# Optimization experiments

Hardware: AMD Instinct MI355X
Metric: run time of the kernel (lower is better)

Reference implementation:

```python
import jax, jax.numpy as jnp
import numpy as np

S, B, I, H = 512, 8192, 3, 5  # seq, batch, input_size, hidden_size


def _uniform(key, shape, bound):
    return jax.random.uniform(key, shape, jnp.float32, -bound, bound)


def setup_inputs() -> dict:
    key = jax.random.key(0)
    ks = jax.random.split(key, 17)
    bound = 1.0 / np.sqrt(H)
    inp = {"x": jax.random.normal(ks[0], (S, B, I), jnp.float32)}
    # layer 0: in=I ; layer 1: in=2H (concat of both directions). Suffix 'r' = reverse direction.
    specs = [
        ("l0", I), ("l0r", I), ("l1", 2 * H), ("l1r", 2 * H),
    ]
    ki = 1
    for name, din in specs:
        inp[f"w_ih_{name}"] = _uniform(ks[ki], (4 * H, din), bound); ki += 1
        inp[f"w_hh_{name}"] = _uniform(ks[ki], (4 * H, H), bound); ki += 1
        inp[f"b_ih_{name}"] = _uniform(ks[ki], (4 * H,), bound); ki += 1
        inp[f"b_hh_{name}"] = _uniform(ks[ki], (4 * H,), bound); ki += 1
    return inp


def _lstm_dir(x, w_ih, w_hh, b_ih, b_hh, reverse):
    """Single-direction LSTM over x [S,B,Din] -> (hs [S,B,H], h_T [B,H], c_T [B,H])."""
    xs = x[::-1] if reverse else x
    # Precompute input contributions for all timesteps in one big matmul.
    gx = jnp.einsum('sbi,gi->sbg', xs, w_ih) + b_ih + b_hh  # [S,B,4H]
    h0 = jnp.zeros((x.shape[1], H), x.dtype)
    c0 = jnp.zeros((x.shape[1], H), x.dtype)

    def step(carry, g):
        h, c = carry
        g = g + h @ w_hh.T  # [B,4H]
        i, f, gg, o = jnp.split(g, 4, axis=-1)  # PyTorch gate order: i,f,g,o
        i = jax.nn.sigmoid(i)
        f = jax.nn.sigmoid(f)
        gg = jnp.tanh(gg)
        o = jax.nn.sigmoid(o)
        c = f * c + i * gg
        h = o * jnp.tanh(c)
        return (h, c), h

    (hT, cT), hs = jax.lax.scan(step, (h0, c0), gx)
    if reverse:
        hs = hs[::-1]
    return hs, hT, cT


def reference(x,
              w_ih_l0, w_hh_l0, b_ih_l0, b_hh_l0,
              w_ih_l0r, w_hh_l0r, b_ih_l0r, b_hh_l0r,
              w_ih_l1, w_hh_l1, b_ih_l1, b_hh_l1,
              w_ih_l1r, w_hh_l1r, b_ih_l1r, b_hh_l1r):
    # Layer 0 (bidirectional)
    hs0f, h0f, c0f = _lstm_dir(x, w_ih_l0, w_hh_l0, b_ih_l0, b_hh_l0, False)
    hs0b, h0b, c0b = _lstm_dir(x, w_ih_l0r, w_hh_l0r, b_ih_l0r, b_hh_l0r, True)
    out0 = jnp.concatenate([hs0f, hs0b], axis=-1)  # [S,B,2H]
    # Layer 1 (bidirectional) consumes concat of both directions
    hs1f, h1f, c1f = _lstm_dir(out0, w_ih_l1, w_hh_l1, b_ih_l1, b_hh_l1, False)
    hs1b, h1b, c1b = _lstm_dir(out0, w_ih_l1r, w_hh_l1r, b_ih_l1r, b_hh_l1r, True)
    output = jnp.concatenate([hs1f, hs1b], axis=-1)  # [S,B,2H]
    # PyTorch h_n/c_n layout: [num_layers*num_directions, B, H] ordered (l0 fwd, l0 bwd, l1 fwd, l1 bwd)
    h_n = jnp.stack([h0f, h0b, h1f, h1b], axis=0)
    c_n = jnp.stack([c0f, c0b, c1f, c1b], axis=0)
    return output, h_n, c_n
```

## Files before the change

kernel.cpp:

```cpp
#include <hip/hip_runtime.h>


constexpr int S_ = 512;
constexpr int B_ = 8192;
constexpr int NROW = 16384;

constexpr float L2E  = 1.4426950408889634f;
constexpr float T2E  = 2.8853900817779268f;
constexpr float IT2E = 0.34657359027997264f;

typedef _Float16 v2h __attribute__((ext_vector_type(2)));

__device__ __forceinline__ float dot2h(v2h a, v2h b, float c) {
#if __has_builtin(__builtin_amdgcn_fdot2)
    return __builtin_amdgcn_fdot2(a, b, c, false);
#else
    return fmaf((float)a[0], (float)b[0], fmaf((float)a[1], (float)b[1], c));
#endif
}

__device__ __forceinline__ float rcp_(float x) { return __builtin_amdgcn_rcpf(x); }

__device__ __forceinline__ float exp2_(float x) {
#if __has_builtin(__builtin_amdgcn_exp2f)
    return __builtin_amdgcn_exp2f(x);
#else
    return exp2f(x);
#endif
}

__device__ __forceinline__ void sbar() { __builtin_amdgcn_sched_barrier(0); }

__device__ __forceinline__ float bperm(int bidx, float v) {
    return __int_as_float(__builtin_amdgcn_ds_bpermute(bidx, __float_as_int(v)));
}

__device__ __forceinline__ unsigned pkh(float a, float b) {
    auto t = __builtin_amdgcn_cvt_pkrtz(a, b);
    unsigned q; __builtin_memcpy(&q, &t, 4); return q;
}

__global__ __launch_bounds__(64) __attribute__((amdgpu_waves_per_eu(1, 2)))
void lstm_layer0(
    const float* __restrict__ x,
    const float* __restrict__ wih_f, const float* __restrict__ whh_f,
    const float* __restrict__ bih_f, const float* __restrict__ bhh_f,
    const float* __restrict__ wih_r, const float* __restrict__ whh_r,
    const float* __restrict__ bih_r, const float* __restrict__ bhh_r,
    unsigned short* __restrict__ ws,
    float* __restrict__ outbase)
{
    const int l64 = threadIdx.x & 63;
    int r = l64 / 5; r = (r > 11) ? 11 : r;
    const int u   = l64 - r * 5;
    const int uc  = (u < 5) ? u : 4;
    const int gid = blockIdx.x * 12 + r;
    const bool valid = gid < NROW;
    const int dir = (gid >> 13) & 1;
    const int b   = gid & 8191;
    const bool stw = valid && (u < 3);
    const bool st  = valid && (u < 5);

    int bidx[5];
#pragma unroll
    for (int k = 0; k < 5; k++) bidx[k] = (r * 5 + k) * 4;

    const float* __restrict__ wih = dir ? wih_r : wih_f;
    const float* __restrict__ whh = dir ? whh_r : whh_f;
    const float* __restrict__ bih = dir ? bih_r : bih_f;
    const float* __restrict__ bhh = dir ? bhh_r : bhh_f;

    const int rows[4] = {uc, 5 + uc, 10 + uc, 15 + uc};
    const float scl[4] = {-L2E, -L2E, T2E, -L2E};
    float WX[4][3], WH[4][5], BS[4];
#pragma unroll
    for (int gi = 0; gi < 4; gi++) {
        const int rr = rows[gi]; const float sc = scl[gi];
#pragma unroll
        for (int i = 0; i < 3; i++) WX[gi][i] = wih[rr * 3 + i] * sc;
#pragma unroll
        for (int k = 0; k < 5; k++) WH[gi][k] = whh[rr * 5 + k] * sc;
        BS[gi] = (bih[rr] + bhh[rr]) * sc;
    }

    float h[5] = {0.f, 0.f, 0.f, 0.f, 0.f};
    float cp = 0.f, hu_last = 0.f;

    const int t0 = dir ? (S_ - 1) : 0;
    const float* xp = x + ((size_t)t0 * B_ + b) * 3;
    unsigned short* wp = ws + (size_t)dir * ((size_t)S_ * B_ * 6)
                            + ((size_t)t0 * B_ + b) * 6;
    const ptrdiff_t xst = dir ? -(ptrdiff_t)3 * B_ : (ptrdiff_t)3 * B_;
    const ptrdiff_t wst = dir ? -(ptrdiff_t)6 * B_ : (ptrdiff_t)6 * B_;

    auto step = [&](const float (&xin)[3], unsigned short* wpp) {
        float a0 = BS[0], a1 = BS[1], a2 = BS[2], a3 = BS[3];
#pragma unroll
        for (int i = 0; i < 3; i++) {
            a0 = fmaf(WX[0][i], xin[i], a0);
            a1 = fmaf(WX[1][i], xin[i], a1);
            a2 = fmaf(WX[2][i], xin[i], a2);
            a3 = fmaf(WX[3][i], xin[i], a3);
        }
#pragma unroll
        for (int k = 0; k < 5; k++) {
            a0 = fmaf(WH[0][k], h[k], a0);
            a1 = fmaf(WH[1][k], h[k], a1);
            a2 = fmaf(WH[2][k], h[k], a2);
            a3 = fmaf(WH[3][k], h[k], a3);
        }
        const float ig = rcp_(1.0f + exp2_(a0));
        const float fg = rcp_(1.0f + exp2_(a1));
        const float g2 = fmaf(-2.0f * T2E, rcp_(1.0f + exp2_(a2)), T2E);
        const float og = rcp_(1.0f + exp2_(a3));
        cp = fmaf(fg, cp, ig * g2);
        const float th = fmaf(-2.0f, rcp_(1.0f + exp2_(cp)), 1.0f);
        const float hu = og * th;
        hu_last = hu;
#pragma unroll
        for (int k = 0; k < 5; k++) h[k] = bperm(bidx[k], hu);
        const unsigned q0 = pkh(h[0], h[1]);
        const unsigned q1 = pkh(h[2], h[3]);
        const unsigned q2 = pkh(h[4], 0.0f);
        unsigned qs = q0;
        qs = (u == 1) ? q1 : qs;
        qs = (u == 2) ? q2 : qs;
        if (stw) ((unsigned*)wpp)[u] = qs;
    };

    auto ld = [&](float (&buf)[3]) {
        __builtin_memcpy(&buf[0], xp, 12);
        xp += xst;
        sbar();
    };

    float x0[3], x1[3], x2[3], x3[3], x4[3], x5[3], x6[3], x7[3];
    ld(x0); ld(x1); ld(x2); ld(x3); ld(x4); ld(x5); ld(x6); ld(x7);

#pragma unroll 1
    for (int s = 0; s < S_ - 8; s += 8) {
        step(x0, wp); wp += wst; ld(x0);
        step(x1, wp); wp += wst; ld(x1);
        step(x2, wp); wp += wst; ld(x2);
        step(x3, wp); wp += wst; ld(x3);
        step(x4, wp); wp += wst; ld(x4);
        step(x5, wp); wp += wst; ld(x5);
        step(x6, wp); wp += wst; ld(x6);
        step(x7, wp); wp += wst; ld(x7);
    }
    step(x0, wp); wp += wst;
    step(x1, wp); wp += wst;
    step(x2, wp); wp += wst;
    step(x3, wp); wp += wst;
    step(x4, wp); wp += wst;
    step(x5, wp); wp += wst;
    step(x6, wp); wp += wst;
    step(x7, wp);

    const size_t OUTE = (size_t)S_ * B_ * 10;
    float* hn = outbase + OUTE + ((size_t)dir * B_ + b) * 5;
    float* cn = hn + (size_t)4 * B_ * 5;
    if (st) { hn[uc] = hu_last; cn[uc] = cp * IT2E; }
}

__global__ __launch_bounds__(64) __attribute__((amdgpu_waves_per_eu(1, 2)))
void lstm_layer1(
    const unsigned short* __restrict__ ws,
    const float* __restrict__ wih_f, const float* __restrict__ whh_f,
    const float* __restrict__ bih_f, const float* __restrict__ bhh_f,
    const float* __restrict__ wih_r, const float* __restrict__ whh_r,
    const float* __restrict__ bih_r, const float* __restrict__ bhh_r,
    float* __restrict__ outbase)
{
    const int l64 = threadIdx.x & 63;
    int r = l64 / 5; r = (r > 11) ? 11 : r;
    const int u   = l64 - r * 5;
    const int uc  = (u < 5) ? u : 4;
    const int gid = blockIdx.x * 12 + r;
    const bool valid = gid < NROW;
    const int dir = (gid >> 13) & 1;
    const int b   = gid & 8191;
    const bool st = valid && (u < 5);

    int bidx[5];
#pragma unroll
    for (int k = 0; k < 5; k++) bidx[k] = (r * 5 + k) * 4;

    const float* __restrict__ wih = dir ? wih_r : wih_f;
    const float* __restrict__ whh = dir ? whh_r : whh_f;
    const float* __restrict__ bih = dir ? bih_r : bih_f;
    const float* __restrict__ bhh = dir ? bhh_r : bhh_f;

    const int rows[4] = {uc, 5 + uc, 10 + uc, 15 + uc};
    const float scl[4] = {-L2E, -L2E, T2E, -L2E};
    v2h WX[4][6];
    float WH[4][5], BS[4];
#pragma unroll
    for (int gi = 0; gi < 4; gi++) {
        const int rr = rows[gi]; const float sc = scl[gi];
#pragma unroll
        for (int p = 0; p < 6; p++) {
            const int i0 = (p < 3) ? 2 * p : 2 * p - 1;
            const bool pad = (p == 2) || (p == 5);
            const float w0 = wih[rr * 10 + i0] * sc;
            const float w1 = pad ? 0.f : wih[rr * 10 + i0 + 1] * sc;
            WX[gi][p] = (v2h){(_Float16)w0, (_Float16)w1};
        }
#pragma unroll
        for (int k = 0; k < 5; k++) WH[gi][k] = whh[rr * 5 + k] * sc;
        BS[gi] = (bih[rr] + bhh[rr]) * sc;
    }

    float h[5] = {0.f, 0.f, 0.f, 0.f, 0.f};
    float cp = 0.f, hu_last = 0.f;

    const int t0 = dir ? (S_ - 1) : 0;
    const unsigned short* rpf = ws + ((size_t)t0 * B_ + b) * 6;
    const unsigned short* rpb = rpf + (size_t)S_ * B_ * 6;
    float* op = outbase + ((size_t)t0 * B_ + b) * 10 + dir * 5;
    const ptrdiff_t rst = dir ? -(ptrdiff_t)6 * B_ : (ptrdiff_t)6 * B_;
    const ptrdiff_t ost = dir ? -(ptrdiff_t)10 * B_ : (ptrdiff_t)10 * B_;

    auto step = [&](const v2h (&xin)[6], float* opp) {
        float a0 = BS[0], a1 = BS[1], a2 = BS[2], a3 = BS[3];
#pragma unroll
        for (int p = 0; p < 6; p++) {
            a0 = dot2h(xin[p], WX[0][p], a0);
            a1 = dot2h(xin[p], WX[1][p], a1);
            a2 = dot2h(xin[p], WX[2][p], a2);
            a3 = dot2h(xin[p], WX[3][p], a3);
        }
#pragma unroll
        for (int k = 0; k < 5; k++) {
            a0 = fmaf(WH[0][k], h[k], a0);
            a1 = fmaf(WH[1][k], h[k], a1);
            a2 = fmaf(WH[2][k], h[k], a2);
            a3 = fmaf(WH[3][k], h[k], a3);
        }
        const float ig = rcp_(1.0f + exp2_(a0));
        const float fg = rcp_(1.0f + exp2_(a1));
        const float g2 = fmaf(-2.0f * T2E, rcp_(1.0f + exp2_(a2)), T2E);
        const float og = rcp_(1.0f + exp2_(a3));
        cp = fmaf(fg, cp, ig * g2);
        const float th = fmaf(-2.0f, rcp_(1.0f + exp2_(cp)), 1.0f);
        const float hu = og * th;
        hu_last = hu;
        if (st) opp[u] = hu;
#pragma unroll
        for (int k = 0; k < 5; k++) h[k] = bperm(bidx[k], hu);
    };

    auto ld = [&](v2h (&buf)[6]) {
        __builtin_memcpy(&buf[0], rpf, 12);
        __builtin_memcpy(&buf[3], rpb, 12);
        rpf += rst; rpb += rst;
        sbar();
    };

    v2h x0[6], x1[6], x2[6], x3[6];
    ld(x0); ld(x1); ld(x2); ld(x3);

#pragma unroll 1
    for (int s = 0; s < S_ - 4; s += 4) {
        step(x0, op); op += ost; ld(x0);
        step(x1, op); op += ost; ld(x1);
        step(x2, op); op += ost; ld(x2);
        step(x3, op); op += ost; ld(x3);
    }
    step(x0, op); op += ost;
    step(x1, op); op += ost;
    step(x2, op); op += ost;
    step(x3, op);

    const size_t OUTE = (size_t)S_ * B_ * 10;
    float* hn = outbase + OUTE + ((size_t)(2 + dir) * B_ + b) * 5;
    float* cn = hn + (size_t)4 * B_ * 5;
    if (st) { hn[uc] = hu_last; cn[uc] = cp * IT2E; }
}

extern "C" void kernel_launch(void* const* d_in, const int* in_sizes, int n_in,
                              void* d_out, int out_size, void* d_ws, size_t ws_size,
                              hipStream_t stream) {
    const float* x       = (const float*)d_in[0];
    const float* wih_l0  = (const float*)d_in[1];
    const float* whh_l0  = (const float*)d_in[2];
    const float* bih_l0  = (const float*)d_in[3];
    const float* bhh_l0  = (const float*)d_in[4];
    const float* wih_l0r = (const float*)d_in[5];
    const float* whh_l0r = (const float*)d_in[6];
    const float* bih_l0r = (const float*)d_in[7];
    const float* bhh_l0r = (const float*)d_in[8];
    const float* wih_l1  = (const float*)d_in[9];
    const float* whh_l1  = (const float*)d_in[10];
    const float* bih_l1  = (const float*)d_in[11];
    const float* bhh_l1  = (const float*)d_in[12];
    const float* wih_l1r = (const float*)d_in[13];
    const float* whh_l1r = (const float*)d_in[14];
    const float* bih_l1r = (const float*)d_in[15];
    const float* bhh_l1r = (const float*)d_in[16];

    float* out = (float*)d_out;
    unsigned short* ws = (unsigned short*)d_ws;

    dim3 grid(1366), block(64);
    lstm_layer0<<<grid, block, 0, stream>>>(x,
        wih_l0, whh_l0, bih_l0, bhh_l0,
        wih_l0r, whh_l0r, bih_l0r, bhh_l0r,
        ws, out);
    lstm_layer1<<<grid, block, 0, stream>>>(ws,
        wih_l1, whh_l1, bih_l1, bhh_l1,
        wih_l1r, whh_l1r, bih_l1r, bhh_l1r,
        out);
}
```

Before: 325.2 us.

## Restructure layer-1 LSTM to one lane per sequence with LDS-paired direction outputs

The layer-1 kernel now gives each lane a full batch element in one direction, computing all 20 gates itself in packed fp16 dot products, instead of spreading 5 hidden units across lanes with bpermute exchanges every step. Forward and reverse lanes for the same batch element sit in the same wave. Each lane stashes its first-half hidden states in LDS so that, during the second half, it can write full 10-float output rows that combine its own and its partner's values. This removes per-step cross-lane shuffles and scattered 4-byte stores, at the cost of far fewer waves (256 blocks), heavy register pressure, and fp16 rounding of the recurrent state and of the outputs taken from the partner lane.

```diff
diff --git a/kernel.cpp b/kernel.cpp
--- a/kernel.cpp
+++ b/kernel.cpp
@@ -5,11 +5,14 @@
 constexpr int B_ = 8192;
 constexpr int NROW = 16384;
 
+constexpr int TLR = 252;
+
 constexpr float L2E  = 1.4426950408889634f;
 constexpr float T2E  = 2.8853900817779268f;
 constexpr float IT2E = 0.34657359027997264f;
 
 typedef _Float16 v2h __attribute__((ext_vector_type(2)));
+typedef unsigned u32;
 
 __device__ __forceinline__ float dot2h(v2h a, v2h b, float c) {
 #if __has_builtin(__builtin_amdgcn_fdot2)
@@ -34,10 +37,22 @@
 __device__ __forceinline__ float bperm(int bidx, float v) {
     return __int_as_float(__builtin_amdgcn_ds_bpermute(bidx, __float_as_int(v)));
 }
+__device__ __forceinline__ u32 bpermu(int bidx, u32 v) {
+    return (u32)__builtin_amdgcn_ds_bpermute(bidx, (int)v);
+}
 
 __device__ __forceinline__ unsigned pkh(float a, float b) {
     auto t = __builtin_amdgcn_cvt_pkrtz(a, b);
     unsigned q; __builtin_memcpy(&q, &t, 4); return q;
+}
+
+__device__ __forceinline__ unsigned short f2h(float x) {
+    _Float16 h = (_Float16)x;
+    unsigned short s; __builtin_memcpy(&s, &h, 2); return s;
+}
+
+__device__ __forceinline__ float h2f(unsigned short s) {
+    _Float16 h; __builtin_memcpy(&h, &s, 2); return (float)h;
 }
 
 __global__ __launch_bounds__(64) __attribute__((amdgpu_waves_per_eu(1, 2)))
@@ -163,7 +178,7 @@
     if (st) { hn[uc] = hu_last; cn[uc] = cp * IT2E; }
 }
 
-__global__ __launch_bounds__(64) __attribute__((amdgpu_waves_per_eu(1, 2)))
+__global__ __launch_bounds__(64) __attribute__((amdgpu_waves_per_eu(1)))
 void lstm_layer1(
     const unsigned short* __restrict__ ws,
     const float* __restrict__ wih_f, const float* __restrict__ whh_f,
@@ -172,110 +187,173 @@
     const float* __restrict__ bih_r, const float* __restrict__ bhh_r,
     float* __restrict__ outbase)
 {
+    __shared__ u32           ltA[TLR * 64];
+    __shared__ u32           ltB[TLR * 64];
+    __shared__ unsigned short ltC[TLR * 64];
+
     const int l64 = threadIdx.x & 63;
-    int r = l64 / 5; r = (r > 11) ? 11 : r;
-    const int u   = l64 - r * 5;
-    const int uc  = (u < 5) ? u : 4;
-    const int gid = blockIdx.x * 12 + r;
-    const bool valid = gid < NROW;
-    const int dir = (gid >> 13) & 1;
-    const int b   = gid & 8191;
-    const bool st = valid && (u < 5);
-
-    int bidx[5];
-#pragma unroll
-    for (int k = 0; k < 5; k++) bidx[k] = (r * 5 + k) * 4;
+    const int dir = l64 >> 5;
+    const int b   = (int)blockIdx.x * 32 + (l64 & 31);
+    const int pli = (l64 ^ 32);
+    const int pswz = pli * 4;
 
     const float* __restrict__ wih = dir ? wih_r : wih_f;
     const float* __restrict__ whh = dir ? whh_r : whh_f;
     const float* __restrict__ bih = dir ? bih_r : bih_f;
     const float* __restrict__ bhh = dir ? bhh_r : bhh_f;
 
-    const int rows[4] = {uc, 5 + uc, 10 + uc, 15 + uc};
-    const float scl[4] = {-L2E, -L2E, T2E, -L2E};
-    v2h WX[4][6];
-    float WH[4][5], BS[4];
-#pragma unroll
-    for (int gi = 0; gi < 4; gi++) {
-        const int rr = rows[gi]; const float sc = scl[gi];
-#pragma unroll
-        for (int p = 0; p < 6; p++) {
-            const int i0 = (p < 3) ? 2 * p : 2 * p - 1;
-            const bool pad = (p == 2) || (p == 5);
-            const float w0 = wih[rr * 10 + i0] * sc;
-            const float w1 = pad ? 0.f : wih[rr * 10 + i0 + 1] * sc;
-            WX[gi][p] = (v2h){(_Float16)w0, (_Float16)w1};
-        }
-#pragma unroll
-        for (int k = 0; k < 5; k++) WH[gi][k] = whh[rr * 5 + k] * sc;
-        BS[gi] = (bih[rr] + bhh[rr]) * sc;
-    }
-
-    float h[5] = {0.f, 0.f, 0.f, 0.f, 0.f};
-    float cp = 0.f, hu_last = 0.f;
+    v2h  WX[20][5];
+    v2h  WHp[20][3];
+    float BS[20];
+#pragma unroll
+    for (int j = 0; j < 20; j++) {
+        const float sc = (j >= 10 && j < 15) ? T2E : -L2E;
+#pragma unroll
+        for (int q = 0; q < 5; q++) {
+            WX[j][q] = (v2h){(_Float16)(wih[j * 10 + 2 * q] * sc),
+                             (_Float16)(wih[j * 10 + 2 * q + 1] * sc)};
+        }
+        WHp[j][0] = (v2h){(_Float16)(whh[j * 5 + 0] * sc),
+                          (_Float16)(whh[j * 5 + 1] * sc)};
+        WHp[j][1] = (v2h){(_Float16)(whh[j * 5 + 2] * sc),
+                          (_Float16)(whh[j * 5 + 3] * sc)};
+        WHp[j][2] = (v2h){(_Float16)(whh[j * 5 + 4] * sc), (_Float16)0.0f};
+        BS[j] = (bih[j] + bhh[j]) * sc;
+    }
+
+    float h[5]  = {0.f, 0.f, 0.f, 0.f, 0.f};
+    float cp[5] = {0.f, 0.f, 0.f, 0.f, 0.f};
+    u32 hv01 = 0, hv23 = 0, hv4 = 0;
 
     const int t0 = dir ? (S_ - 1) : 0;
-    const unsigned short* rpf = ws + ((size_t)t0 * B_ + b) * 6;
-    const unsigned short* rpb = rpf + (size_t)S_ * B_ * 6;
-    float* op = outbase + ((size_t)t0 * B_ + b) * 10 + dir * 5;
+    const unsigned short* rp0 = ws + ((size_t)t0 * B_ + b) * 6;
+    const unsigned short* rp1 = rp0 + (size_t)S_ * B_ * 6;
     const ptrdiff_t rst = dir ? -(ptrdiff_t)6 * B_ : (ptrdiff_t)6 * B_;
+    float* op = outbase + ((size_t)(dir ? 255 : 256) * B_ + b) * 10;
     const ptrdiff_t ost = dir ? -(ptrdiff_t)10 * B_ : (ptrdiff_t)10 * B_;
 
-    auto step = [&](const v2h (&xin)[6], float* opp) {
-        float a0 = BS[0], a1 = BS[1], a2 = BS[2], a3 = BS[3];
-#pragma unroll
-        for (int p = 0; p < 6; p++) {
-            a0 = dot2h(xin[p], WX[0][p], a0);
-            a1 = dot2h(xin[p], WX[1][p], a1);
-            a2 = dot2h(xin[p], WX[2][p], a2);
-            a3 = dot2h(xin[p], WX[3][p], a3);
-        }
-#pragma unroll
-        for (int k = 0; k < 5; k++) {
-            a0 = fmaf(WH[0][k], h[k], a0);
-            a1 = fmaf(WH[1][k], h[k], a1);
-            a2 = fmaf(WH[2][k], h[k], a2);
-            a3 = fmaf(WH[3][k], h[k], a3);
-        }
-        const float ig = rcp_(1.0f + exp2_(a0));
-        const float fg = rcp_(1.0f + exp2_(a1));
-        const float g2 = fmaf(-2.0f * T2E, rcp_(1.0f + exp2_(a2)), T2E);
-        const float og = rcp_(1.0f + exp2_(a3));
-        cp = fmaf(fg, cp, ig * g2);
-        const float th = fmaf(-2.0f, rcp_(1.0f + exp2_(cp)), 1.0f);
-        const float hu = og * th;
-        hu_last = hu;
-        if (st) opp[u] = hu;
-#pragma unroll
-        for (int k = 0; k < 5; k++) h[k] = bperm(bidx[k], hu);
-    };
-
-    auto ld = [&](v2h (&buf)[6]) {
-        __builtin_memcpy(&buf[0], rpf, 12);
-        __builtin_memcpy(&buf[3], rpb, 12);
-        rpf += rst; rpb += rst;
+    auto ld = [&](u32 (&P)[6]) {
+        __builtin_memcpy(&P[0], rp0, 12);
+        __builtin_memcpy(&P[3], rp1, 12);
+        rp0 += rst; rp1 += rst;
         sbar();
     };
 
-    v2h x0[6], x1[6], x2[6], x3[6];
-    ld(x0); ld(x1); ld(x2); ld(x3);
+    auto core = [&](const u32 (&P)[6]) {
+        v2h xin[5];
+        const u32 xc = (P[2] & 0xFFFFu) | (P[3] << 16);
+        const u32 xd = (P[3] >> 16)     | (P[4] << 16);
+        const u32 xe = (P[4] >> 16)     | (P[5] << 16);
+        __builtin_memcpy(&xin[0], &P[0], 4);
+        __builtin_memcpy(&xin[1], &P[1], 4);
+        __builtin_memcpy(&xin[2], &xc, 4);
+        __builtin_memcpy(&xin[3], &xd, 4);
+        __builtin_memcpy(&xin[4], &xe, 4);
+        v2h hp0, hp1, hp2;
+        __builtin_memcpy(&hp0, &hv01, 4);
+        __builtin_memcpy(&hp1, &hv23, 4);
+        __builtin_memcpy(&hp2, &hv4, 4);
+        float g[20];
+#pragma unroll
+        for (int j = 0; j < 20; j++) {
+            float t = BS[j];
+#pragma unroll
+            for (int q = 0; q < 5; q++) t = dot2h(xin[q], WX[j][q], t);
+            t = dot2h(hp0, WHp[j][0], t);
+            t = dot2h(hp1, WHp[j][1], t);
+            t = dot2h(hp2, WHp[j][2], t);
+            const float e = rcp_(1.0f + exp2_(t));
+            g[j] = (j >= 10 && j < 15) ? fmaf(-2.0f * T2E, e, T2E) : e;
+        }
+#pragma unroll
+        for (int u = 0; u < 5; u++) {
+            cp[u] = fmaf(g[5 + u], cp[u], g[u] * g[10 + u]);
+            const float th = fmaf(-2.0f, rcp_(1.0f + exp2_(cp[u])), 1.0f);
+            h[u] = g[15 + u] * th;
+        }
+        hv01 = pkh(h[0], h[1]);
+        hv23 = pkh(h[2], h[3]);
+        hv4  = pkh(h[4], 0.0f);
+    };
+
+    auto outw = [&](u32 p01, u32 p23, u32 p4s) {
+        float pv[5];
+        pv[0] = h2f((unsigned short)(p01 & 0xFFFF));
+        pv[1] = h2f((unsigned short)(p01 >> 16));
+        pv[2] = h2f((unsigned short)(p23 & 0xFFFF));
+        pv[3] = h2f((unsigned short)(p23 >> 16));
+        pv[4] = h2f((unsigned short)(p4s & 0xFFFF));
+        float buf[10];
+#pragma unroll
+        for (int u = 0; u < 5; u++) {
+            buf[u]     = dir ? pv[u] : h[u];
+            buf[5 + u] = dir ? h[u]  : pv[u];
+        }
+        __builtin_memcpy(op, buf, 40);
+        op += ost;
+    };
+
+    auto s1L = [&](u32 (&P)[6], int t) {
+        core(P); ld(P);
+        ltA[t * 64 + l64] = hv01;
+        ltB[t * 64 + l64] = hv23;
+        ltC[t * 64 + l64] = (unsigned short)(hv4 & 0xFFFF);
+    };
+    u32 sv01[4], sv23[4], sv4[4];
+    auto s1R = [&](u32 (&P)[6], int k) {
+        core(P); ld(P);
+        sv01[k] = hv01; sv23[k] = hv23; sv4[k] = hv4;
+    };
+    auto s2R = [&](u32 (&P)[6], int k) {
+        core(P); ld(P);
+        outw(sv01[k], sv23[k], sv4[k]);
+    };
+    auto s2L = [&](u32 (&P)[6], int t) {
+        const int tau = 511 - t;
+        const u32 p01 = ltA[tau * 64 + pli];
+        const u32 p23 = ltB[tau * 64 + pli];
+        const u32 p4  = (u32)ltC[tau * 64 + pli];
+        core(P); ld(P);
+        outw(p01, p23, p4);
+    };
+    auto s2Ln = [&](u32 (&P)[6], int t) {
+        const int tau = 511 - t;
+        const u32 p01 = ltA[tau * 64 + pli];
+        const u32 p23 = ltB[tau * 64 + pli];
+        const u32 p4  = (u32)ltC[tau * 64 + pli];
+        core(P);
+        outw(p01, p23, p4);
+    };
+
+    u32 X0[6], X1[6], X2[6], X3[6];
+    ld(X0); ld(X1); ld(X2); ld(X3);
 
 #pragma unroll 1
-    for (int s = 0; s < S_ - 4; s += 4) {
-        step(x0, op); op += ost; ld(x0);
-        step(x1, op); op += ost; ld(x1);
-        step(x2, op); op += ost; ld(x2);
-        step(x3, op); op += ost; ld(x3);
-    }
-    step(x0, op); op += ost;
-    step(x1, op); op += ost;
-    step(x2, op); op += ost;
-    step(x3, op);
+    for (int t = 0; t < TLR; t += 4) {
+        s1L(X0, t); s1L(X1, t + 1); s1L(X2, t + 2); s1L(X3, t + 3);
+    }
+    s1R(X0, 0); s1R(X1, 1); s1R(X2, 2); s1R(X3, 3);
+#pragma unroll
+    for (int k = 0; k < 4; k++) {
+        sv01[k] = bpermu(pswz, sv01[k]);
+        sv23[k] = bpermu(pswz, sv23[k]);
+        sv4[k]  = bpermu(pswz, sv4[k]);
+    }
+    s2R(X0, 3); s2R(X1, 2); s2R(X2, 1); s2R(X3, 0);
+#pragma unroll 1
+    for (int t = 260; t < 508; t += 4) {
+        s2L(X0, t); s2L(X1, t + 1); s2L(X2, t + 2); s2L(X3, t + 3);
+    }
+    s2Ln(X0, 508); s2Ln(X1, 509); s2Ln(X2, 510); s2Ln(X3, 511);
 
     const size_t OUTE = (size_t)S_ * B_ * 10;
     float* hn = outbase + OUTE + ((size_t)(2 + dir) * B_ + b) * 5;
     float* cn = hn + (size_t)4 * B_ * 5;
-    if (st) { hn[uc] = hu_last; cn[uc] = cp * IT2E; }
+    float hb[5], cb[5];
+#pragma unroll
+    for (int u = 0; u < 5; u++) { hb[u] = h[u]; cb[u] = cp[u] * IT2E; }
+    __builtin_memcpy(hn, hb, 20);
+    __builtin_memcpy(cn, cb, 20);
 }
 
 extern "C" void kernel_launch(void* const* d_in, const int* in_sizes, int n_in,
@@ -302,12 +380,13 @@
     float* out = (float*)d_out;
     unsigned short* ws = (unsigned short*)d_ws;
 
-    dim3 grid(1366), block(64);
-    lstm_layer0<<<grid, block, 0, stream>>>(x,
+    dim3 grid0(1366), block(64);
+    lstm_layer0<<<grid0, block, 0, stream>>>(x,
         wih_l0, whh_l0, bih_l0, bhh_l0,
         wih_l0r, whh_l0r, bih_l0r, bhh_l0r,
         ws, out);
-    lstm_layer1<<<grid, block, 0, stream>>>(ws,
+    dim3 grid1(256);
+    lstm_layer1<<<grid1, block, 0, stream>>>(ws,
         wih_l1, whh_l1, bih_l1, bhh_l1,
         wih_l1r, whh_l1r, bih_l1r, bhh_l1r,
         out);
```

New measurement: 590.8 us. 81.7% more time.
